# Optimization experiments

Measured on AMD Instinct MI355X. Metric: run time of the kernel, lower is better.

## Reference

```python
import jax, jax.numpy as jnp
import numpy as np

N = 50000          # nodes
E_RAND = 800000    # random edges
E = E_RAND + N     # + self loops -> 850000
F_IN = 256         # nembed
F_HID = 64         # nhid
H = 8              # nheads
NCLASS = 40
ALPHA = 0.2        # leakyrelu slope


def setup_inputs() -> dict:
    key = jax.random.key(0)
    ks = jax.random.split(key, 8)
    x = jax.random.normal(ks[0], (N, F_IN), dtype=jnp.float32)
    # random edges + self loops (guarantees every row-sum > 0, like adj + I)
    er = jax.random.randint(ks[1], (2, E_RAND), 0, N, dtype=jnp.int32)
    loops = jnp.tile(jnp.arange(N, dtype=jnp.int32)[None, :], (2, 1))
    edge_index = jnp.concatenate([er, loops], axis=1)  # [2, E]
    # per-head attention params (xavier-ish scale)
    W = jax.random.normal(ks[2], (H, F_IN, F_HID), dtype=jnp.float32) * (1.0 / np.sqrt(F_IN))
    a = jax.random.normal(ks[3], (H, 2 * F_HID), dtype=jnp.float32) * 0.1
    Wo = jax.random.normal(ks[4], (H * F_HID, F_HID), dtype=jnp.float32) * (1.0 / np.sqrt(H * F_HID))
    ao = jax.random.normal(ks[5], (2 * F_HID,), dtype=jnp.float32) * 0.1
    mlp_w = jax.random.normal(ks[6], (NCLASS, F_HID), dtype=jnp.float32) * 0.05
    mlp_b = jnp.zeros((NCLASS,), dtype=jnp.float32)
    return {"x": x, "edge_index": edge_index, "W": W, "a": a,
            "Wo": Wo, "ao": ao, "mlp_w": mlp_w, "mlp_b": mlp_b}


def _leaky(v):
    return jnp.where(v > 0, v, ALPHA * v)


def _spgat_layer(x, W, a, src, dst, n):
    """pyGAT SpGraphAttentionLayer (eval mode, dropout = identity).
    out[i] = sum_{e: src=i} exp(-leakyrelu(a.[h_src;h_dst])) * h[dst] / rowsum_i
    """
    h = x @ W                         # [N, D]
    D = W.shape[1]
    s_src = h @ a[:D]                 # [N]
    s_dst = h @ a[D:]                 # [N]
    # per-edge unnormalized attention (note the -exp(leaky) of original sp impl)
    e = jnp.exp(-_leaky(s_src[src] + s_dst[dst]))          # [E]
    rowsum = jax.ops.segment_sum(e, src, num_segments=n)   # [N]
    num = jax.ops.segment_sum(e[:, None] * h[dst], src, num_segments=n)  # [N, D]
    return num / rowsum[:, None]


def reference(x, edge_index, W, a, Wo, ao, mlp_w, mlp_b):
    src, dst = edge_index[0], edge_index[1]
    # multi-head attention, concat=True -> elu inside each head
    heads = [jax.nn.elu(_spgat_layer(x, W[i], a[i], src, dst, N)) for i in range(H)]
    xc = jnp.concatenate(heads, axis=1)                     # [N, H*F_HID]
    # dropout (eval) = identity
    xo = jax.nn.elu(_spgat_layer(xc, Wo, ao, src, dst, N))  # [N, F_HID]
    return xo @ mlp_w.T + mlp_b                             # [N, NCLASS]
```

## Files before the change

kernel.cpp:

```cpp
#include <hip/hip_runtime.h>

#define NN 50000
#define HH 8
#define ALPHA 0.2f
#define NPAD 50048

typedef short short8 __attribute__((ext_vector_type(8)));
typedef float f32x4 __attribute__((ext_vector_type(4)));

__device__ __forceinline__ float elu_f(float x) {
  return x > 0.f ? x : __expf(x) - 1.f;
}

__device__ __forceinline__ unsigned short f2bf(float f) {
  unsigned int u = __float_as_uint(f);
  unsigned int r = (u + 0x7fffu + ((u >> 16) & 1u)) >> 16;
  return (unsigned short)r;
}

__global__ void cvt_all_kernel(const float* __restrict__ x, unsigned short* __restrict__ xb,
                               const float* __restrict__ W, unsigned short* __restrict__ Wtc,
                               const float* __restrict__ Wo, unsigned short* __restrict__ Wot,
                               int* __restrict__ cnt, int N) {
  int tid = blockIdx.x * 256 + threadIdx.x;
  int n4x = NPAD * 64;
  if (tid < n4x) {
    int row = tid >> 6;
    ushort4 o;
    if (row < N) {
      float4 v = ((const float4*)x)[tid];
      o.x = f2bf(v.x); o.y = f2bf(v.y); o.z = f2bf(v.z); o.w = f2bf(v.w);
    } else {
      o.x = o.y = o.z = o.w = 0;
    }
    ((ushort4*)xb)[tid] = o;
    return;
  }
  int t1 = tid - n4x;
  if (t1 < 512 * 256) {
    int c = t1 >> 8, k = t1 & 255;
    int h = c >> 6, cc = c & 63;
    Wtc[t1] = f2bf(W[((size_t)h * 256 + k) * 64 + cc]);
    return;
  }
  int t2 = t1 - 512 * 256;
  if (t2 < 64 * 512) {
    int c = t2 >> 9, k = t2 & 511;
    Wot[t2] = f2bf(Wo[(size_t)k * 64 + c]);
    return;
  }
  int t3 = t2 - 64 * 512;
  if (t3 < N) cnt[t3] = 0;
}

__global__ void hist_kernel(const int* __restrict__ src, int* __restrict__ cnt, int E) {
  int e = blockIdx.x * blockDim.x + threadIdx.x;
  if (e < E) atomicAdd(&cnt[src[e]], 1);
}

__global__ __launch_bounds__(1024) void scan_blocks_kernel(const int* __restrict__ cnt,
    int* __restrict__ tmp, int* __restrict__ bsum, int n) {
  __shared__ int sh[1024];
  int i = blockIdx.x * 1024 + threadIdx.x;
  int v = (i < n) ? cnt[i] : 0;
  sh[threadIdx.x] = v;
  __syncthreads();
  for (int off = 1; off < 1024; off <<= 1) {
    int t = (threadIdx.x >= off) ? sh[threadIdx.x - off] : 0;
    __syncthreads();
    sh[threadIdx.x] += t;
    __syncthreads();
  }
  if (i < n) tmp[i] = sh[threadIdx.x] - v;
  if (threadIdx.x == 1023) bsum[blockIdx.x] = sh[1023];
}

__global__ __launch_bounds__(1024) void scan_apply_kernel(const int* __restrict__ tmp,
    const int* __restrict__ bsum, int* __restrict__ row_ptr, int* __restrict__ nxt,
    int n, int E, int nb) {
  __shared__ int boff_sh;
  if (threadIdx.x < 64) {
    int L = threadIdx.x;
    int v = (L < nb && L < (int)blockIdx.x) ? bsum[L] : 0;
#pragma unroll
    for (int off = 1; off < 64; off <<= 1) v += __shfl_xor(v, off, 64);
    if (L == 0) boff_sh = v;
  }
  __syncthreads();
  int i = blockIdx.x * 1024 + threadIdx.x;
  if (i < n) {
    int s = tmp[i] + boff_sh;
    row_ptr[i] = s;
    nxt[i] = s;
  }
  if (i == 0) row_ptr[n] = E;
}

__global__ void scatter_kernel(const int* __restrict__ src, const int* __restrict__ dst,
                               int* __restrict__ nxt, int* __restrict__ col, int E) {
  int e = blockIdx.x * blockDim.x + threadIdx.x;
  if (e < E) {
    int p = atomicAdd(&nxt[src[e]], 1);
    col[p] = dst[e];
  }
}

__global__ __launch_bounds__(256) void mfma_gemm1_kernel(
    const unsigned short* __restrict__ A, const unsigned short* __restrict__ Wtc,
    const float* __restrict__ Aatt, unsigned short* __restrict__ Cout,
    float* __restrict__ ss, float* __restrict__ sd, int N) {
  __shared__ unsigned short As[128][40];
  __shared__ unsigned short Bs[128][40];
  int m0 = blockIdx.x * 128;
  int c0 = blockIdx.y * 128;
  int w = threadIdx.x >> 6, L = threadIdx.x & 63;
  int quad = L >> 4, l16 = L & 15;
  int wr = w >> 1, wc = w & 1;
  int y = blockIdx.y * 2 + wc;

  f32x4 acc[4][4];
#pragma unroll
  for (int mt = 0; mt < 4; ++mt)
#pragma unroll
    for (int nt = 0; nt < 4; ++nt) acc[mt][nt] = (f32x4)(0.f);

  int sr0 = threadIdx.x >> 2;
  int sk0 = (threadIdx.x & 3) << 3;

  for (int k0 = 0; k0 < 256; k0 += 32) {
    __syncthreads();
    *(uint4*)&As[sr0][sk0]      = *(const uint4*)(A + (size_t)(m0 + sr0) * 256 + k0 + sk0);
    *(uint4*)&As[sr0 + 64][sk0] = *(const uint4*)(A + (size_t)(m0 + sr0 + 64) * 256 + k0 + sk0);
    *(uint4*)&Bs[sr0][sk0]      = *(const uint4*)(Wtc + (size_t)(c0 + sr0) * 256 + k0 + sk0);
    *(uint4*)&Bs[sr0 + 64][sk0] = *(const uint4*)(Wtc + (size_t)(c0 + sr0 + 64) * 256 + k0 + sk0);
    __syncthreads();

    short8 af[4], bf[4];
#pragma unroll
    for (int mt = 0; mt < 4; ++mt)
      af[mt] = *(const short8*)&As[wr * 64 + mt * 16 + l16][quad * 8];
#pragma unroll
    for (int nt = 0; nt < 4; ++nt)
      bf[nt] = *(const short8*)&Bs[wc * 64 + nt * 16 + l16][quad * 8];
#pragma unroll
    for (int mt = 0; mt < 4; ++mt)
#pragma unroll
      for (int nt = 0; nt < 4; ++nt)
        acc[mt][nt] = __builtin_amdgcn_mfma_f32_16x16x32_bf16(af[mt], bf[nt], acc[mt][nt], 0, 0, 0);
  }

  float as[4], ad[4];
#pragma unroll
  for (int nt = 0; nt < 4; ++nt) {
    as[nt] = Aatt[y * 128 + l16 + 16 * nt];
    ad[nt] = Aatt[y * 128 + 64 + l16 + 16 * nt];
  }
#pragma unroll
  for (int mt = 0; mt < 4; ++mt) {
#pragma unroll
    for (int reg = 0; reg < 4; ++reg) {
      int row = m0 + wr * 64 + mt * 16 + quad * 4 + reg;
      float p = 0.f, q = 0.f;
#pragma unroll
      for (int nt = 0; nt < 4; ++nt) {
        p += acc[mt][nt][reg] * as[nt];
        q += acc[mt][nt][reg] * ad[nt];
      }
#pragma unroll
      for (int off = 1; off < 16; off <<= 1) {
        p += __shfl_xor(p, off, 64);
        q += __shfl_xor(q, off, 64);
      }
      if (l16 == 0 && row < N) {
        ss[(size_t)row * 8 + y] = p;
        sd[(size_t)row * 8 + y] = q;
      }
      if (row < N) {
#pragma unroll
        for (int nt = 0; nt < 4; ++nt)
          Cout[(size_t)row * 512 + y * 64 + l16 + 16 * nt] = f2bf(acc[mt][nt][reg]);
      }
    }
  }
}

__global__ __launch_bounds__(256) void mfma_gemm2_kernel(
    const unsigned short* __restrict__ A, const unsigned short* __restrict__ Bt,
    const float* __restrict__ Aatt, unsigned short* __restrict__ Cout,
    float* __restrict__ ss, float* __restrict__ sd, int N) {
  __shared__ unsigned short Bs[64][520];
  unsigned short* stage = &Bs[0][0];
  {
    for (int c = threadIdx.x; c < 4096; c += 256) {
      int n = c >> 6;
      int kq = (c & 63) << 3;
      *(uint4*)&Bs[n][kq] = *(const uint4*)(Bt + (size_t)n * 512 + kq);
    }
  }
  __syncthreads();

  int w = threadIdx.x >> 6, L = threadIdx.x & 63;
  int quad = L >> 4, l16 = L & 15;
  int m0 = blockIdx.x * 64;
  int myrow = m0 + w * 16 + l16;
  const unsigned short* Ar = A + (size_t)myrow * 512 + quad * 8;

  f32x4 acc[4];
#pragma unroll
  for (int nt = 0; nt < 4; ++nt) acc[nt] = (f32x4)(0.f);

  short8 a_cur = *(const short8*)(Ar);
  for (int k0 = 0; k0 < 512; k0 += 32) {
    short8 a_nxt;
    if (k0 + 32 < 512) a_nxt = *(const short8*)(Ar + k0 + 32);
#pragma unroll
    for (int nt = 0; nt < 4; ++nt) {
      short8 b = *(const short8*)&Bs[l16 + 16 * nt][k0 + quad * 8];
      acc[nt] = __builtin_amdgcn_mfma_f32_16x16x32_bf16(a_cur, b, acc[nt], 0, 0, 0);
    }
    a_cur = a_nxt;
  }

  float as[4], ad[4];
#pragma unroll
  for (int nt = 0; nt < 4; ++nt) {
    as[nt] = Aatt[l16 + 16 * nt];
    ad[nt] = Aatt[64 + l16 + 16 * nt];
  }
#pragma unroll
  for (int reg = 0; reg < 4; ++reg) {
    float p = 0.f, q = 0.f;
#pragma unroll
    for (int nt = 0; nt < 4; ++nt) {
      p += acc[nt][reg] * as[nt];
      q += acc[nt][reg] * ad[nt];
    }
#pragma unroll
    for (int off = 1; off < 16; off <<= 1) {
      p += __shfl_xor(p, off, 64);
      q += __shfl_xor(q, off, 64);
    }
    int row = m0 + w * 16 + quad * 4 + reg;
    if (l16 == 0 && row < N) { ss[row] = p; sd[row] = q; }
  }

  __syncthreads();
#pragma unroll
  for (int reg = 0; reg < 4; ++reg) {
    int lrow = w * 16 + quad * 4 + reg;
#pragma unroll
    for (int nt = 0; nt < 4; ++nt)
      stage[lrow * 72 + l16 + 16 * nt] = f2bf(acc[nt][reg]);
  }
  __syncthreads();
#pragma unroll
  for (int i = 0; i < 2; ++i) {
    int idx = threadIdx.x + 256 * i;
    int row = idx >> 3;
    int c8 = (idx & 7) << 3;
    if (m0 + row < N) {
      uint4 v = *(const uint4*)&stage[row * 72 + c8];
      *(uint4*)(Cout + ((size_t)(m0 + row)) * 64 + c8) = v;
    }
  }
}

__global__ __launch_bounds__(256) void agg1_kernel(const unsigned short* __restrict__ table,
    const float* __restrict__ ss, const float* __restrict__ sd,
    const int* __restrict__ row_ptr, const int* __restrict__ col,
    unsigned short* __restrict__ xc, int N) {
  int bid = blockIdx.x;
  int r8 = bid & 7;
  int p = r8 >> 2;
  int nb = ((bid >> 3) << 2) | (r8 & 3);
  int wid = threadIdx.x >> 6, L = threadIdx.x & 63;
  int n = nb * 4 + wid;
  if (n >= N) return;
  int hq = L >> 4;
  int h = p * 4 + hq;
  int el = L & 15;
  float ssn = ss[n * 8 + h];
  int k0 = row_ptr[n], deg = row_ptr[n + 1] - k0;
  float acc[4] = {0.f, 0.f, 0.f, 0.f};
  float rs = 0.f;
  const char* tb = (const char*)table + p * 512;

  for (int c0 = 0; c0 < deg; c0 += 64) {
    int j = c0 + L;
    int d_l = (j < deg) ? col[k0 + j] : 0;
    int m = min(64, deg - c0);
    for (int g = 0; g < m; g += 16) {
      int eoff = g + el;
      int de = __shfl(d_l, eoff, 64);
      float s = ssn + sd[(size_t)de * 8 + h];
      float e = __expf(-fmaxf(s, ALPHA * s));
      if (eoff >= m) e = 0.f;
      rs += e;
      int gm = min(16, m - g);
      uint2 rv[16];
#pragma unroll
      for (int t = 0; t < 16; ++t) {
        if (t < gm) {
          int dg = __builtin_amdgcn_readlane(d_l, g + t);
          rv[t] = *(const uint2*)(tb + (size_t)dg * 1024 + L * 8);
        }
      }
#pragma unroll
      for (int t = 0; t < 16; ++t) {
        if (t < gm) {
          float ew = __shfl(e, (hq << 4) + t, 64);
          acc[0] += ew * __uint_as_float(rv[t].x << 16);
          acc[1] += ew * __uint_as_float(rv[t].x & 0xffff0000u);
          acc[2] += ew * __uint_as_float(rv[t].y << 16);
          acc[3] += ew * __uint_as_float(rv[t].y & 0xffff0000u);
        }
      }
    }
  }
  rs += __shfl_xor(rs, 1, 64);
  rs += __shfl_xor(rs, 2, 64);
  rs += __shfl_xor(rs, 4, 64);
  rs += __shfl_xor(rs, 8, 64);
  float inv = 1.f / rs;
  ushort4 pk;
  pk.x = f2bf(elu_f(acc[0] * inv));
  pk.y = f2bf(elu_f(acc[1] * inv));
  pk.z = f2bf(elu_f(acc[2] * inv));
  pk.w = f2bf(elu_f(acc[3] * inv));
  *(ushort4*)(xc + (size_t)n * 512 + p * 256 + L * 4) = pk;
}

__global__ __launch_bounds__(256) void agg2_final_kernel(const unsigned short* __restrict__ table,
    const float* __restrict__ ss, const float* __restrict__ sd,
    const int* __restrict__ row_ptr, const int* __restrict__ col,
    const float* __restrict__ mlp_w, const float* __restrict__ mlp_b,
    float* __restrict__ out, int N) {
  __shared__ float osh[4][68];
  int wid = threadIdx.x >> 6, L = threadIdx.x & 63;
  int n = blockIdx.x * 4 + wid;
  bool act = (n < N);
  float o = 0.f;
  if (act) {
    float ssn = ss[n];
    int k0 = row_ptr[n], deg = row_ptr[n + 1] - k0;
    float acc = 0.f, rs = 0.f;
    const char* base = (const char*)table;
    for (int c0 = 0; c0 < deg; c0 += 64) {
      int j = c0 + L;
      int d_l = 0;
      float e_l = 0.f;
      if (j < deg) {
        d_l = col[k0 + j];
        float s = ssn + sd[d_l];
        e_l = __expf(-fmaxf(s, ALPHA * s));
      }
      rs += e_l;
      int m = min(64, deg - c0);
      int off_l = d_l << 7;
      for (int g = 0; g < m; g += 16) {
        int gm = min(16, m - g);
        unsigned hv[16];
#pragma unroll
        for (int t = 0; t < 16; ++t) {
          if (t < gm) {
            int so = __builtin_amdgcn_readlane(off_l, g + t);
            hv[t] = *(const unsigned short*)(base + so + L * 2);
          }
        }
#pragma unroll
        for (int t = 0; t < 16; ++t) {
          if (t < gm) {
            float ew = __uint_as_float(
                (unsigned)__builtin_amdgcn_readlane(__float_as_uint(e_l), g + t));
            acc += ew * __uint_as_float(hv[t] << 16);
          }
        }
      }
    }
#pragma unroll
    for (int off = 1; off < 64; off <<= 1) rs += __shfl_xor(rs, off, 64);
    o = elu_f(acc / rs);
  }
  osh[wid][L] = o;
  __syncthreads();

  if (act && L < 40) {
    const float* wrow = mlp_w + L * 64;
    float acc = mlp_b[L];
    const float4* op = (const float4*)osh[wid];
#pragma unroll
    for (int j = 0; j < 16; ++j) {
      float4 wv = *(const float4*)(wrow + j * 4);
      float4 ov = op[j];
      acc += ov.x * wv.x + ov.y * wv.y + ov.z * wv.z + ov.w * wv.w;
    }
    out[(size_t)n * 40 + L] = acc;
  }
}

extern "C" void kernel_launch(void* const* d_in, const int* in_sizes, int n_in,
                              void* d_out, int out_size, void* d_ws, size_t ws_size,
                              hipStream_t stream) {
  (void)n_in; (void)out_size; (void)ws_size;
  const float* x  = (const float*)d_in[0];
  const int*   ei = (const int*)d_in[1];
  const float* W  = (const float*)d_in[2];
  const float* a  = (const float*)d_in[3];
  const float* Wo = (const float*)d_in[4];
  const float* ao = (const float*)d_in[5];
  const float* mw = (const float*)d_in[6];
  const float* mb = (const float*)d_in[7];
  float* out = (float*)d_out;

  const int N = NN;
  const int E = in_sizes[1] / 2;
  const int* src = ei;
  const int* dst = ei + E;

  char* ws = (char*)d_ws;
  size_t off = 0;
  auto alloc = [&](size_t bytes) {
    char* p = ws + off;
    off = (off + bytes + 255) & ~(size_t)255;
    return p;
  };
  unsigned short* xb  = (unsigned short*)alloc((size_t)NPAD * 256 * 2);
  unsigned short* Wtc = (unsigned short*)alloc((size_t)512 * 256 * 2);
  unsigned short* Wot = (unsigned short*)alloc((size_t)64 * 512 * 2);
  unsigned short* h1b = (unsigned short*)alloc((size_t)N * 512 * 2);
  float* ss1     = (float*)alloc((size_t)N * 8 * 4);
  float* sd1     = (float*)alloc((size_t)N * 8 * 4);
  unsigned short* xc = (unsigned short*)alloc((size_t)NPAD * 512 * 2);
  unsigned short* h2b = (unsigned short*)alloc((size_t)N * 64 * 2);
  float* ss2     = (float*)alloc((size_t)N * 4);
  float* sd2     = (float*)alloc((size_t)N * 4);
  int*   row_ptr = (int*)  alloc((size_t)(N + 1) * 4);
  int*   nxt     = (int*)  alloc((size_t)N * 4);
  int*   cnt     = (int*)  alloc((size_t)N * 4);
  int*   tmp     = (int*)  alloc((size_t)N * 4);
  int*   bsum    = (int*)  alloc(64 * 4);
  int*   colv    = (int*)  alloc((size_t)E * 4);

  int eb = (E + 255) / 256;
  int nb1024 = (N + 1023) / 1024;
  int cvt_total = NPAD * 64 + 512 * 256 + 64 * 512 + N;

  hipLaunchKernelGGL(cvt_all_kernel, dim3((cvt_total + 255) / 256), dim3(256), 0, stream,
                     x, xb, W, Wtc, Wo, Wot, cnt, N);

  hipLaunchKernelGGL(hist_kernel, dim3(eb), dim3(256), 0, stream, src, cnt, E);
  hipLaunchKernelGGL(scan_blocks_kernel, dim3(nb1024), dim3(1024), 0, stream, cnt, tmp, bsum, N);
  hipLaunchKernelGGL(scan_apply_kernel, dim3(nb1024), dim3(1024), 0, stream,
                     tmp, bsum, row_ptr, nxt, N, E, nb1024);
  hipLaunchKernelGGL(scatter_kernel, dim3(eb), dim3(256), 0, stream, src, dst, nxt, colv, E);

  hipLaunchKernelGGL(mfma_gemm1_kernel, dim3(NPAD / 128, 4), dim3(256), 0, stream,
                     xb, Wtc, a, h1b, ss1, sd1, N);
  hipLaunchKernelGGL(agg1_kernel, dim3(2 * ((N + 3) / 4)), dim3(256), 0, stream,
                     h1b, ss1, sd1, row_ptr, colv, xc, N);

  hipLaunchKernelGGL(mfma_gemm2_kernel, dim3(NPAD / 64), dim3(256), 0, stream,
                     xc, Wot, ao, h2b, ss2, sd2, N);
  hipLaunchKernelGGL(agg2_final_kernel, dim3((N + 3) / 4), dim3(256), 0, stream,
                     h2b, ss2, sd2, row_ptr, colv, mw, mb, out, N);
}
```

Baseline: 468.2 us.

## Fuse scan passes, merge edge scatter into GEMM1 launch, stage MLP weights in LDS

The two-pass block scan becomes a single kernel. Each block computes its base offset by summing all earlier counts directly instead of reading separate block sums. The edge scatter runs as extra blocks at the front of the first GEMM launch, so the atomic scatter can overlap with the MFMA tiles. The final MLP weights and bias are staged in padded shared memory per block, which saves two launches but adds redundant prefix summing and per-block weight loading.

```diff
diff --git a/kernel.cpp b/kernel.cpp
--- a/kernel.cpp
+++ b/kernel.cpp
@@ -58,65 +58,68 @@
   if (e < E) atomicAdd(&cnt[src[e]], 1);
 }
 
-__global__ __launch_bounds__(1024) void scan_blocks_kernel(const int* __restrict__ cnt,
-    int* __restrict__ tmp, int* __restrict__ bsum, int n) {
+__global__ __launch_bounds__(1024) void scan_fused_kernel(const int* __restrict__ cnt,
+    int* __restrict__ row_ptr, int* __restrict__ nxt, int n, int E) {
   __shared__ int sh[1024];
-  int i = blockIdx.x * 1024 + threadIdx.x;
+  __shared__ int wsum[16];
+  __shared__ int base_sh;
+  int bid = blockIdx.x;
+  int i = (bid << 10) + threadIdx.x;
   int v = (i < n) ? cnt[i] : 0;
+
+  int lim = bid << 10;
+  int s = 0;
+  for (int q = threadIdx.x; q < lim; q += 1024) s += cnt[q];
+#pragma unroll
+  for (int off = 1; off < 64; off <<= 1) s += __shfl_xor(s, off, 64);
+  if ((threadIdx.x & 63) == 0) wsum[threadIdx.x >> 6] = s;
   sh[threadIdx.x] = v;
   __syncthreads();
+  if (threadIdx.x == 0) {
+    int t = 0;
+#pragma unroll
+    for (int j = 0; j < 16; ++j) t += wsum[j];
+    base_sh = t;
+  }
   for (int off = 1; off < 1024; off <<= 1) {
     int t = (threadIdx.x >= off) ? sh[threadIdx.x - off] : 0;
     __syncthreads();
     sh[threadIdx.x] += t;
     __syncthreads();
   }
-  if (i < n) tmp[i] = sh[threadIdx.x] - v;
-  if (threadIdx.x == 1023) bsum[blockIdx.x] = sh[1023];
-}
-
-__global__ __launch_bounds__(1024) void scan_apply_kernel(const int* __restrict__ tmp,
-    const int* __restrict__ bsum, int* __restrict__ row_ptr, int* __restrict__ nxt,
-    int n, int E, int nb) {
-  __shared__ int boff_sh;
-  if (threadIdx.x < 64) {
-    int L = threadIdx.x;
-    int v = (L < nb && L < (int)blockIdx.x) ? bsum[L] : 0;
-#pragma unroll
-    for (int off = 1; off < 64; off <<= 1) v += __shfl_xor(v, off, 64);
-    if (L == 0) boff_sh = v;
-  }
-  __syncthreads();
-  int i = blockIdx.x * 1024 + threadIdx.x;
   if (i < n) {
-    int s = tmp[i] + boff_sh;
-    row_ptr[i] = s;
-    nxt[i] = s;
+    int r = base_sh + sh[threadIdx.x] - v;
+    row_ptr[i] = r;
+    nxt[i] = r;
   }
   if (i == 0) row_ptr[n] = E;
 }
 
-__global__ void scatter_kernel(const int* __restrict__ src, const int* __restrict__ dst,
-                               int* __restrict__ nxt, int* __restrict__ col, int E) {
-  int e = blockIdx.x * blockDim.x + threadIdx.x;
-  if (e < E) {
-    int p = atomicAdd(&nxt[src[e]], 1);
-    col[p] = dst[e];
-  }
-}
-
-__global__ __launch_bounds__(256) void mfma_gemm1_kernel(
+__global__ __launch_bounds__(256) void scatter_gemm1_kernel(
+    const int* __restrict__ src, const int* __restrict__ dst,
+    int* __restrict__ nxt, int* __restrict__ colv, int E, int eb,
     const unsigned short* __restrict__ A, const unsigned short* __restrict__ Wtc,
     const float* __restrict__ Aatt, unsigned short* __restrict__ Cout,
     float* __restrict__ ss, float* __restrict__ sd, int N) {
   __shared__ unsigned short As[128][40];
   __shared__ unsigned short Bs[128][40];
-  int m0 = blockIdx.x * 128;
-  int c0 = blockIdx.y * 128;
+
+  if (blockIdx.x < (unsigned)eb) {
+    int e = blockIdx.x * 256 + threadIdx.x;
+    if (e < E) {
+      int p = atomicAdd(&nxt[src[e]], 1);
+      colv[p] = dst[e];
+    }
+    return;
+  }
+
+  int tile = blockIdx.x - eb;
+  int m0 = (tile >> 2) * 128;
+  int c0 = (tile & 3) * 128;
   int w = threadIdx.x >> 6, L = threadIdx.x & 63;
   int quad = L >> 4, l16 = L & 15;
   int wr = w >> 1, wc = w & 1;
-  int y = blockIdx.y * 2 + wc;
+  int y = (tile & 3) * 2 + wc;
 
   f32x4 acc[4][4];
 #pragma unroll
@@ -335,7 +338,13 @@
     const int* __restrict__ row_ptr, const int* __restrict__ col,
     const float* __restrict__ mlp_w, const float* __restrict__ mlp_b,
     float* __restrict__ out, int N) {
+  __shared__ float wsh[40 * 65];
+  __shared__ float bsh[40];
   __shared__ float osh[4][68];
+  for (int i = threadIdx.x; i < 40 * 64; i += 256) wsh[(i >> 6) * 65 + (i & 63)] = mlp_w[i];
+  if (threadIdx.x < 40) bsh[threadIdx.x] = mlp_b[threadIdx.x];
+  __syncthreads();
+
   int wid = threadIdx.x >> 6, L = threadIdx.x & 63;
   int n = blockIdx.x * 4 + wid;
   bool act = (n < N);
@@ -383,17 +392,12 @@
   }
   osh[wid][L] = o;
   __syncthreads();
-
   if (act && L < 40) {
-    const float* wrow = mlp_w + L * 64;
-    float acc = mlp_b[L];
-    const float4* op = (const float4*)osh[wid];
-#pragma unroll
-    for (int j = 0; j < 16; ++j) {
-      float4 wv = *(const float4*)(wrow + j * 4);
-      float4 ov = op[j];
-      acc += ov.x * wv.x + ov.y * wv.y + ov.z * wv.z + ov.w * wv.w;
-    }
+    const float* wr = wsh + L * 65;
+    const float* orow = osh[wid];
+    float acc = bsh[L];
+#pragma unroll
+    for (int j = 0; j < 64; ++j) acc += orow[j] * wr[j];
     out[(size_t)n * 40 + L] = acc;
   }
 }
@@ -437,25 +441,24 @@
   int*   row_ptr = (int*)  alloc((size_t)(N + 1) * 4);
   int*   nxt     = (int*)  alloc((size_t)N * 4);
   int*   cnt     = (int*)  alloc((size_t)N * 4);
-  int*   tmp     = (int*)  alloc((size_t)N * 4);
-  int*   bsum    = (int*)  alloc(64 * 4);
   int*   colv    = (int*)  alloc((size_t)E * 4);
 
   int eb = (E + 255) / 256;
   int nb1024 = (N + 1023) / 1024;
   int cvt_total = NPAD * 64 + 512 * 256 + 64 * 512 + N;
+  int gtiles = (NPAD / 128) * 4;
 
   hipLaunchKernelGGL(cvt_all_kernel, dim3((cvt_total + 255) / 256), dim3(256), 0, stream,
                      x, xb, W, Wtc, Wo, Wot, cnt, N);
 
   hipLaunchKernelGGL(hist_kernel, dim3(eb), dim3(256), 0, stream, src, cnt, E);
-  hipLaunchKernelGGL(scan_blocks_kernel, dim3(nb1024), dim3(1024), 0, stream, cnt, tmp, bsum, N);
-  hipLaunchKernelGGL(scan_apply_kernel, dim3(nb1024), dim3(1024), 0, stream,
-                     tmp, bsum, row_ptr, nxt, N, E, nb1024);
-  hipLaunchKernelGGL(scatter_kernel, dim3(eb), dim3(256), 0, stream, src, dst, nxt, colv, E);
-
-  hipLaunchKernelGGL(mfma_gemm1_kernel, dim3(NPAD / 128, 4), dim3(256), 0, stream,
+  hipLaunchKernelGGL(scan_fused_kernel, dim3(nb1024), dim3(1024), 0, stream,
+                     cnt, row_ptr, nxt, N, E);
+
+  hipLaunchKernelGGL(scatter_gemm1_kernel, dim3(eb + gtiles), dim3(256), 0, stream,
+                     src, dst, nxt, colv, E, eb,
                      xb, Wtc, a, h1b, ss1, sd1, N);
+
   hipLaunchKernelGGL(agg1_kernel, dim3(2 * ((N + 3) / 4)), dim3(256), 0, stream,
                      h1b, ss1, sd1, row_ptr, colv, xc, N);
 
```

After: 442.1 us. -5.6%, faster.
